# Kernel tuning notes

Hardware: AMD Instinct MI355X
Metric: run time of the kernel (lower is better)

Reference implementation:

```python
import jax, jax.numpy as jnp
import numpy as np

N_NODES = 50000
N_EDGES = 800000
D = 128          # embed_dim
H = 8            # heads
C = D // H       # per-head channels
F = 512          # ff_hidden_dim
LN_EPS = 1e-5
NEG_SLOPE = 0.2  # PyG GATConv default negative_slope


def _layernorm(x, g, b):
    mu = jnp.mean(x, axis=-1, keepdims=True)
    var = jnp.mean(jnp.square(x - mu), axis=-1, keepdims=True)
    return (x - mu) * jax.lax.rsqrt(var + LN_EPS) * g + b


def _gat_conv(x, edge_index, W, att_src, att_dst, bias):
    # PyG GATConv (concat=True, add_self_loops=True, shared lin for src/dst)
    N = x.shape[0]
    xl = (x @ W.T).reshape(N, H, C)                 # [N,H,C]
    a_s = jnp.sum(xl * att_src, axis=-1)            # [N,H]
    a_d = jnp.sum(xl * att_dst, axis=-1)            # [N,H]
    loops = jnp.arange(N)
    src = jnp.concatenate([edge_index[0], loops])   # [E+N]
    dst = jnp.concatenate([edge_index[1], loops])
    e = jax.nn.leaky_relu(a_s[src] + a_d[dst], NEG_SLOPE)  # [E+N,H]
    # segment softmax over incoming edges per destination node
    m = jax.ops.segment_max(e, dst, num_segments=N)
    m = jnp.where(jnp.isfinite(m), m, jnp.zeros_like(m))
    ex = jnp.exp(e - m[dst])
    s = jax.ops.segment_sum(ex, dst, num_segments=N)
    alpha = ex / (s[dst] + 1e-16)                   # [E+N,H]
    msg = xl[src] * alpha[:, :, None]               # [E+N,H,C]
    out = jax.ops.segment_sum(msg, dst, num_segments=N)  # [N,H,C]
    return out.reshape(N, H * C) + bias


def setup_inputs() -> dict:
    key = jax.random.key(0)
    ks = jax.random.split(key, 12)
    sc_d = 1.0 / np.sqrt(D)
    sc_f = 1.0 / np.sqrt(F)
    return {
        "x": jax.random.normal(ks[0], (N_NODES, D), dtype=jnp.float32),
        "virtual_edge_index": jax.random.randint(ks[1], (2, N_EDGES), 0, N_NODES, dtype=jnp.int64),
        "W_gat": jax.random.normal(ks[2], (H * C, D), dtype=jnp.float32) * sc_d,
        "att_src": jax.random.normal(ks[3], (H, C), dtype=jnp.float32) * sc_d,
        "att_dst": jax.random.normal(ks[4], (H, C), dtype=jnp.float32) * sc_d,
        "bias_gat": jnp.zeros((H * C,), dtype=jnp.float32),
        "W1": jax.random.normal(ks[5], (F, D), dtype=jnp.float32) * sc_d,
        "b1": jnp.zeros((F,), dtype=jnp.float32),
        "W2": jax.random.normal(ks[6], (D, F), dtype=jnp.float32) * sc_f,
        "b2": jnp.zeros((D,), dtype=jnp.float32),
        "g1": jnp.ones((D,), dtype=jnp.float32),
        "beta1": jnp.zeros((D,), dtype=jnp.float32),
        "g2": jnp.ones((D,), dtype=jnp.float32),
        "beta2": jnp.zeros((D,), dtype=jnp.float32),
    }


def reference(x, virtual_edge_index, W_gat, att_src, att_dst, bias_gat,
              W1, b1, W2, b2, g1, beta1, g2, beta2):
    h_gat = _gat_conv(x, virtual_edge_index, W_gat, att_src, att_dst, bias_gat)
    h = _layernorm(x + h_gat, g1, beta1)
    h_ff = jax.nn.relu(h @ W1.T + b1) @ W2.T + b2
    return _layernorm(h + h_ff, g2, beta2)
```

## Files before the change

### kernel.cpp

```cpp
#include <hip/hip_runtime.h>
#include <hip/hip_bf16.h>

#define N_NODES 50000
#define N_EDGES 800000
#define N_TOT   850000
#define DIM 128
#define HEADS 8
#define CH 16
#define FF 512
#define LN_EPS 1e-5f
#define NEG_SLOPE 0.2f

typedef __bf16 bf16x8 __attribute__((ext_vector_type(8)));
typedef float f32x4 __attribute__((ext_vector_type(4)));

__device__ __forceinline__ float bfr2f(unsigned short u) {
  return __uint_as_float(((unsigned)u) << 16);
}
__device__ __forceinline__ unsigned short f2bfr(float f) {
  __hip_bfloat16 h = __float2bfloat16(f);
  return *(unsigned short*)&h;
}
__device__ __forceinline__ float bf2f(__hip_bfloat16 h) { return __bfloat162float(h); }
__device__ __forceinline__ __hip_bfloat16 f2bf(float f) { return __float2bfloat16(f); }

__device__ __forceinline__ bf16x8 ldcvt8(const float* __restrict__ p) {
  const float4 a = ((const float4*)p)[0];
  const float4 b = ((const float4*)p)[1];
  bf16x8 r;
  r[0] = (__bf16)a.x; r[1] = (__bf16)a.y; r[2] = (__bf16)a.z; r[3] = (__bf16)a.w;
  r[4] = (__bf16)b.x; r[5] = (__bf16)b.y; r[6] = (__bf16)b.z; r[7] = (__bf16)b.w;
  return r;
}

__device__ __forceinline__ int ld_src(const int* ei, int mode, int e) {
  int v = mode ? ei[2 * e] : ei[e];
  return min(max(v, 0), N_NODES - 1);
}
__device__ __forceinline__ int ld_dst(const int* ei, int mode, int e) {
  int v = mode ? ei[2 * (N_EDGES + e)] : ei[N_EDGES + e];
  return min(max(v, 0), N_NODES - 1);
}
__device__ __forceinline__ int edge_mode(const int* __restrict__ ei) {
  int any = 0;
  for (int k = 1; k < 64; k += 2) any |= ei[k];
  return (any == 0) ? 1 : 0;
}

__device__ __forceinline__ float expleaky(float v) {
  v = v > 0.f ? v : NEG_SLOPE * v;
  return __expf(v);
}

__global__ __launch_bounds__(256) void k_xl(const float* __restrict__ x,
                                            const float* __restrict__ Wg,
                                            const float* __restrict__ att_s,
                                            const float* __restrict__ att_d,
                                            __hip_bfloat16* __restrict__ xl,
                                            float* __restrict__ a_s,
                                            float* __restrict__ a_d,
                                            int* __restrict__ dz) {
  int gid = blockIdx.x * 256 + threadIdx.x;
  if (gid < 100096) dz[gid] = 0;
  int w = gid >> 6;
  if (w >= 3125 * 2) return;
  int l = threadIdx.x & 63, quad = l >> 4, r = l & 15;
  int strip = w >> 1, cc = w & 1;
  f32x4 acc[4];
#pragma unroll
  for (int t = 0; t < 4; ++t) acc[t] = (f32x4){0.f, 0.f, 0.f, 0.f};
  int arow = strip * 16 + r;
  bf16x8 af[4];
#pragma unroll
  for (int kk = 0; kk < 4; ++kk) af[kk] = ldcvt8(x + arow * DIM + kk * 32 + quad * 8);
#pragma unroll
  for (int kk = 0; kk < 4; ++kk) {
    bf16x8 bfr[4];
#pragma unroll
    for (int t = 0; t < 4; ++t)
      bfr[t] = ldcvt8(Wg + (cc * 64 + t * 16 + r) * DIM + kk * 32 + quad * 8);
#pragma unroll
    for (int t = 0; t < 4; ++t)
      acc[t] = __builtin_amdgcn_mfma_f32_16x16x32_bf16(af[kk], bfr[t], acc[t], 0, 0, 0);
  }
  float ats[4], atd[4];
#pragma unroll
  for (int t = 0; t < 4; ++t) {
    ats[t] = att_s[(cc * 4 + t) * CH + r];
    atd[t] = att_d[(cc * 4 + t) * CH + r];
  }
#pragma unroll
  for (int t = 0; t < 4; ++t)
#pragma unroll
    for (int j = 0; j < 4; ++j) {
      int row = strip * 16 + quad * 4 + j;
      int col = cc * 64 + t * 16 + r;
      xl[row * DIM + col] = f2bf(acc[t][j]);
      float vs = acc[t][j] * ats[t];
      float vd = acc[t][j] * atd[t];
      vs += __shfl_xor(vs, 1); vd += __shfl_xor(vd, 1);
      vs += __shfl_xor(vs, 2); vd += __shfl_xor(vd, 2);
      vs += __shfl_xor(vs, 4); vd += __shfl_xor(vd, 4);
      vs += __shfl_xor(vs, 8); vd += __shfl_xor(vd, 8);
      if (r == 0) {
        a_s[row * 8 + cc * 4 + t] = vs;
        a_d[row * 8 + cc * 4 + t] = vd;
      }
    }
}

__global__ __launch_bounds__(256) void k_hist(const int* __restrict__ ei,
                                              const float* __restrict__ W1,
                                              const float* __restrict__ W2,
                                              __hip_bfloat16* __restrict__ wb,
                                              int* __restrict__ deg) {
  int i = blockIdx.x * 256 + threadIdx.x;
  if (i < 65536)        wb[i] = f2bf(W1[i]);
  else if (i < 131072)  wb[i] = f2bf(W2[i - 65536]);
  int m = edge_mode(ei);
  if (i < N_EDGES) atomicAdd(&deg[ld_dst(ei, m, i)], 1);
}

__global__ __launch_bounds__(1024) void k_scan(const int* __restrict__ deg, int* __restrict__ offs) {
  __shared__ int wtot[16];
  __shared__ int wbase[16];
  __shared__ int running_s;
  int tid = threadIdx.x, wv = tid >> 6, ln = tid & 63;
  if (tid == 0) running_s = 0;
  __syncthreads();
  for (int base = 0; base < N_NODES; base += 4096) {
    int i0 = base + tid * 4;
    int v0 = 0, v1 = 0, v2 = 0, v3 = 0;
    if (i0 + 3 < N_NODES) {
      int4 dv = *(const int4*)(deg + i0);
      v0 = dv.x + 1; v1 = dv.y + 1; v2 = dv.z + 1; v3 = dv.w + 1;
    } else {
      if (i0 + 0 < N_NODES) v0 = deg[i0 + 0] + 1;
      if (i0 + 1 < N_NODES) v1 = deg[i0 + 1] + 1;
      if (i0 + 2 < N_NODES) v2 = deg[i0 + 2] + 1;
      if (i0 + 3 < N_NODES) v3 = deg[i0 + 3] + 1;
    }
    int tt = v0 + v1 + v2 + v3;
    int xsc = tt;
#pragma unroll
    for (int off = 1; off < 64; off <<= 1) {
      int t = __shfl_up(xsc, off);
      if (ln >= off) xsc += t;
    }
    if (ln == 63) wtot[wv] = xsc;
    __syncthreads();
    if (wv == 0) {
      int t = (ln < 16) ? wtot[ln] : 0;
#pragma unroll
      for (int off = 1; off < 16; off <<= 1) {
        int u = __shfl_up(t, off);
        if (ln >= off) t += u;
      }
      if (ln < 16) wbase[ln] = t;
    }
    __syncthreads();
    int run0 = running_s;
    int excl = run0 + ((wv == 0) ? 0 : wbase[wv - 1]) + xsc - tt;
    if (i0 + 0 < N_NODES) offs[i0 + 0] = excl;
    excl += v0;
    if (i0 + 1 < N_NODES) offs[i0 + 1] = excl;
    excl += v1;
    if (i0 + 2 < N_NODES) offs[i0 + 2] = excl;
    excl += v2;
    if (i0 + 3 < N_NODES) offs[i0 + 3] = excl;
    __syncthreads();
    if (tid == 1023) running_s = run0 + wbase[15];
  }
  __syncthreads();
  if (tid == 0) offs[N_NODES] = running_s;
}

__global__ __launch_bounds__(256) void k_scatter(const int* __restrict__ ei,
                                                 const int* __restrict__ offs,
                                                 int* __restrict__ fill, int* __restrict__ eid) {
  int e = blockIdx.x * 256 + threadIdx.x;
  if (e < N_NODES) { eid[offs[e]] = e; }
  int m = edge_mode(ei);
  if (e < N_EDGES) {
    int d = ld_dst(ei, m, e);
    int p = offs[d] + 1 + atomicAdd(&fill[d], 1);
    eid[p] = ld_src(ei, m, e);
  }
}

__global__ __launch_bounds__(256) void k_attn(const int* __restrict__ eid, const int* __restrict__ offs,
                                              const float* __restrict__ a_s,
                                              const float* __restrict__ a_d,
                                              const __hip_bfloat16* __restrict__ xl,
                                              const float* __restrict__ x,
                                              const float* __restrict__ bias,
                                              const float* __restrict__ g1,
                                              const float* __restrict__ be1,
                                              __hip_bfloat16* __restrict__ h1out) {
  int wv = threadIdx.x >> 6, l = threadIdx.x & 63;
  int n = blockIdx.x * 4 + wv;
  int start = offs[n], end = offs[n + 1];
  int h8 = l & 7, sl8 = l >> 3;
  int hq = l >> 3;
  float adv = a_d[n * 8 + h8];

  const char* xlb = (const char*)xl;
  int l4 = 4 * l;
  float sme = 0.f;
  float A0 = 0.f, A1 = 0.f;
  int p = start;
  for (; p + 8 <= end; p += 8) {
    int s = eid[p + sl8];
    int boff = s << 8;
    float w = expleaky(a_s[s * 8 + h8] + adv);
    sme += w;
#pragma unroll
    for (int q = 0; q < 8; ++q) {
      int bq = __shfl(boff, q * 8);
      float wq = __shfl(w, q * 8 + hq);
      ushort2 u = *(const ushort2*)(xlb + bq + l4);
      A0 += wq * bfr2f(u.x);
      A1 += wq * bfr2f(u.y);
    }
  }
  int rem = end - p;
  if (rem > 0) {
    int sl = (sl8 < rem) ? sl8 : 0;
    int s = eid[p + sl];
    int boff = s << 8;
    float w = (sl8 < rem) ? expleaky(a_s[s * 8 + h8] + adv) : 0.f;
    sme += w;
    for (int q = 0; q < rem; ++q) {
      int bq = __shfl(boff, q * 8);
      float wq = __shfl(w, q * 8 + hq);
      ushort2 u = *(const ushort2*)(xlb + bq + l4);
      A0 += wq * bfr2f(u.x);
      A1 += wq * bfr2f(u.y);
    }
  }
  sme += __shfl_xor(sme, 8);
  sme += __shfl_xor(sme, 16);
  sme += __shfl_xor(sme, 32);
  float smh = __shfl(sme, hq);
  float inv = 1.f / (smh + 1e-16f);
  float acc0 = A0 * inv;
  float acc1 = A1 * inv;

  float2 xv = *(const float2*)(x + n * DIM + 2 * l);
  float2 bv = *(const float2*)(bias + 2 * l);
  float v0 = acc0 + bv.x + xv.x;
  float v1 = acc1 + bv.y + xv.y;
  float s2 = v0 + v1;
  for (int off = 32; off >= 1; off >>= 1) s2 += __shfl_xor(s2, off);
  float mu = s2 * (1.f / 128.f);
  float d0 = v0 - mu, d1 = v1 - mu;
  float q = d0 * d0 + d1 * d1;
  for (int off = 32; off >= 1; off >>= 1) q += __shfl_xor(q, off);
  float rs = rsqrtf(q * (1.f / 128.f) + LN_EPS);
  float2 gv = *(const float2*)(g1 + 2 * l);
  float2 bev = *(const float2*)(be1 + 2 * l);
  ushort2 o;
  o.x = f2bfr(d0 * rs * gv.x + bev.x);
  o.y = f2bfr(d1 * rs * gv.y + bev.y);
  *(ushort2*)((unsigned short*)h1out + n * DIM + 2 * l) = o;
}

__global__ __launch_bounds__(256) void k_ffn1(const __hip_bfloat16* __restrict__ h1,
                                              const __hip_bfloat16* __restrict__ W1b,
                                              const float* __restrict__ b1,
                                              __hip_bfloat16* __restrict__ hid,
                                              int row_base) {
  int wv = threadIdx.x >> 6, l = threadIdx.x & 63, quad = l >> 4, r = l & 15;
  int blk = blockIdx.x;
  int base = row_base + blk * 32;
  const __bf16* h1b = (const __bf16*)h1;
  const __bf16* w1 = (const __bf16*)W1b;
  int r0 = min(base + r, N_NODES - 1);
  int r1 = min(base + 16 + r, N_NODES - 1);

  bf16x8 bn[2][4];
#pragma unroll
  for (int kk = 0; kk < 4; ++kk) {
    bn[0][kk] = *(const bf16x8*)(h1b + r0 * DIM + kk * 32 + quad * 8);
    bn[1][kk] = *(const bf16x8*)(h1b + r1 * DIM + kk * 32 + quad * 8);
  }
  f32x4 acc1[8][2];
#pragma unroll
  for (int tm = 0; tm < 8; ++tm)
#pragma unroll
    for (int tn = 0; tn < 2; ++tn) acc1[tm][tn] = (f32x4){0.f, 0.f, 0.f, 0.f};
#pragma unroll
  for (int kk = 0; kk < 4; ++kk) {
    bf16x8 wf[8];
#pragma unroll
    for (int tm = 0; tm < 8; ++tm)
      wf[tm] = *(const bf16x8*)(w1 + (wv * 128 + tm * 16 + r) * DIM + kk * 32 + quad * 8);
#pragma unroll
    for (int tm = 0; tm < 8; ++tm) {
      acc1[tm][0] = __builtin_amdgcn_mfma_f32_16x16x32_bf16(wf[tm], bn[0][kk], acc1[tm][0], 0, 0, 0);
      acc1[tm][1] = __builtin_amdgcn_mfma_f32_16x16x32_bf16(wf[tm], bn[1][kk], acc1[tm][1], 0, 0, 0);
    }
  }
  unsigned short* hb = (unsigned short*)hid;
#pragma unroll
  for (int tm = 0; tm < 8; ++tm) {
    int f0 = wv * 128 + tm * 16 + quad * 4;
    float4 bb = *(const float4*)(b1 + f0);
#pragma unroll
    for (int tn = 0; tn < 2; ++tn) {
      ushort4 o;
      o.x = f2bfr(fmaxf(acc1[tm][tn][0] + bb.x, 0.f));
      o.y = f2bfr(fmaxf(acc1[tm][tn][1] + bb.y, 0.f));
      o.z = f2bfr(fmaxf(acc1[tm][tn][2] + bb.z, 0.f));
      o.w = f2bfr(fmaxf(acc1[tm][tn][3] + bb.w, 0.f));
      int idx = ((blk * 2 + tn) * 64 + wv * 16 + tm * 2 + (quad >> 1)) * 128
                + r * 8 + (quad & 1) * 4;
      *(ushort4*)(hb + idx) = o;
    }
  }
}

__global__ __launch_bounds__(256) void k_ffn2(const __hip_bfloat16* __restrict__ hid,
                                              const __hip_bfloat16* __restrict__ W2b,
                                              const float* __restrict__ b2,
                                              const float* __restrict__ g2,
                                              const float* __restrict__ be2,
                                              const __hip_bfloat16* __restrict__ h1,
                                              float* __restrict__ out,
                                              int row_base) {
  __shared__ float ps[4][2][16], pq[4][2][16];
  int wv = threadIdx.x >> 6, l = threadIdx.x & 63, quad = l >> 4, r = l & 15;
  int blk = blockIdx.x;
  int base = row_base + blk * 32;
  const __bf16* w2 = (const __bf16*)W2b;
  const unsigned short* hb = (const unsigned short*)hid;

  f32x4 acc2[2][2];
#pragma unroll
  for (int s = 0; s < 2; ++s)
#pragma unroll
    for (int tn = 0; tn < 2; ++tn) acc2[s][tn] = (f32x4){0.f, 0.f, 0.f, 0.f};

  const unsigned short* a0base = hb + ((blk * 2 + 0) * 64 + quad) * 128 + r * 8;
  const unsigned short* a1base = hb + ((blk * 2 + 1) * 64 + quad) * 128 + r * 8;
  const __bf16* w2base = w2 + (wv * 32 + r) * FF + quad * 8;

#pragma unroll 4
  for (int ka = 0; ka < 16; ++ka) {
    bf16x8 a0 = *(const bf16x8*)(a0base + ka * 512);
    bf16x8 a1 = *(const bf16x8*)(a1base + ka * 512);
    bf16x8 wa0 = *(const bf16x8*)(w2base + ka * 32);
    bf16x8 wa1 = *(const bf16x8*)(w2base + 16 * FF + ka * 32);
    acc2[0][0] = __builtin_amdgcn_mfma_f32_16x16x32_bf16(a0, wa0, acc2[0][0], 0, 0, 0);
    acc2[0][1] = __builtin_amdgcn_mfma_f32_16x16x32_bf16(a0, wa1, acc2[0][1], 0, 0, 0);
    acc2[1][0] = __builtin_amdgcn_mfma_f32_16x16x32_bf16(a1, wa0, acc2[1][0], 0, 0, 0);
    acc2[1][1] = __builtin_amdgcn_mfma_f32_16x16x32_bf16(a1, wa1, acc2[1][1], 0, 0, 0);
  }
#pragma unroll
  for (int s = 0; s < 2; ++s)
#pragma unroll
    for (int tn = 0; tn < 2; ++tn) {
      int col = wv * 32 + tn * 16 + r;
      float b2c = b2[col];
#pragma unroll
      for (int j = 0; j < 4; ++j) {
        int row = min(base + s * 16 + quad * 4 + j, N_NODES - 1);
        acc2[s][tn][j] += b2c + bf2f(h1[row * DIM + col]);
      }
    }
#pragma unroll
  for (int s = 0; s < 2; ++s)
#pragma unroll
    for (int j = 0; j < 4; ++j) {
      float sm = acc2[s][0][j] + acc2[s][1][j];
      float qm = acc2[s][0][j] * acc2[s][0][j] + acc2[s][1][j] * acc2[s][1][j];
      sm += __shfl_xor(sm, 1); sm += __shfl_xor(sm, 2); sm += __shfl_xor(sm, 4); sm += __shfl_xor(sm, 8);
      qm += __shfl_xor(qm, 1); qm += __shfl_xor(qm, 2); qm += __shfl_xor(qm, 4); qm += __shfl_xor(qm, 8);
      if (r == j) { ps[wv][s][quad * 4 + j] = sm; pq[wv][s][quad * 4 + j] = qm; }
    }
  __syncthreads();
#pragma unroll
  for (int s = 0; s < 2; ++s)
#pragma unroll
    for (int j = 0; j < 4; ++j) {
      int row16 = quad * 4 + j;
      float st = (ps[0][s][row16] + ps[1][s][row16]) + (ps[2][s][row16] + ps[3][s][row16]);
      float qt = (pq[0][s][row16] + pq[1][s][row16]) + (pq[2][s][row16] + pq[3][s][row16]);
      float mu = st * (1.f / 128.f);
      float var = qt * (1.f / 128.f) - mu * mu;
      float rs = rsqrtf(var + LN_EPS);
      int grow = base + s * 16 + row16;
      if (grow < N_NODES) {
#pragma unroll
        for (int tn = 0; tn < 2; ++tn) {
          int col = wv * 32 + tn * 16 + r;
          out[grow * DIM + col] = (acc2[s][tn][j] - mu) * rs * g2[col] + be2[col];
        }
      }
    }
}

#define OFF_XL     0u
#define SZ_XL      (N_NODES * DIM * 2u)
#define OFF_AS     (OFF_XL + SZ_XL)
#define SZ_AS      (N_NODES * HEADS * 4u)
#define OFF_AD     (OFF_AS + SZ_AS)
#define OFF_DEG    (OFF_AD + SZ_AS)
#define SZ_DEG     200192u
#define OFF_FILL   (OFF_DEG + SZ_DEG)
#define OFF_OFFS   (OFF_FILL + SZ_DEG)
#define SZ_OFFS    200448u
#define OFF_EID    (OFF_OFFS + SZ_OFFS)
#define SZ_EID     3400192u
#define OFF_H1     (OFF_EID + SZ_EID)
#define SZ_H1      (50016u * DIM * 2u)
#define OFF_WB     (OFF_H1 + SZ_H1)
#define SZ_WB      262144u
#define OFF_HID    (OFF_WB + SZ_WB)
#define SZ_HID_FULL (50016u * FF * 2u)
#define FFN_CHUNK0_BLOCKS 782
#define FFN_CHUNK1_BLOCKS 781
#define FFN_CHUNK0_ROWS   (FFN_CHUNK0_BLOCKS * 32)

extern "C" void kernel_launch(void* const* d_in, const int* in_sizes, int n_in,
                              void* d_out, int out_size, void* d_ws, size_t ws_size,
                              hipStream_t stream) {
  const float* x     = (const float*)d_in[0];
  const int*   ei    = (const int*)d_in[1];
  const float* Wg    = (const float*)d_in[2];
  const float* att_s = (const float*)d_in[3];
  const float* att_d = (const float*)d_in[4];
  const float* bias  = (const float*)d_in[5];
  const float* W1    = (const float*)d_in[6];
  const float* b1    = (const float*)d_in[7];
  const float* W2    = (const float*)d_in[8];
  const float* b2    = (const float*)d_in[9];
  const float* g1    = (const float*)d_in[10];
  const float* be1   = (const float*)d_in[11];
  const float* g2    = (const float*)d_in[12];
  const float* be2   = (const float*)d_in[13];

  char* ws = (char*)d_ws;
  __hip_bfloat16* xl     = (__hip_bfloat16*)(ws + OFF_XL);
  float*          a_s    = (float*)(ws + OFF_AS);
  float*          a_d    = (float*)(ws + OFF_AD);
  int*            deg    = (int*)(ws + OFF_DEG);
  int*            fill   = (int*)(ws + OFF_FILL);
  int*            offs   = (int*)(ws + OFF_OFFS);
  int*            eid    = (int*)(ws + OFF_EID);
  __hip_bfloat16* h1     = (__hip_bfloat16*)(ws + OFF_H1);
  __hip_bfloat16* wbuf   = (__hip_bfloat16*)(ws + OFF_WB);
  __hip_bfloat16* W1b    = wbuf;
  __hip_bfloat16* W2b    = wbuf + 65536;
  __hip_bfloat16* hid    = (__hip_bfloat16*)(ws + OFF_HID);
  float*          out    = (float*)d_out;

  k_xl     <<<1563,  256, 0, stream>>>(x, Wg, att_s, att_d, xl, a_s, a_d, deg);
  k_hist   <<<3125,  256, 0, stream>>>(ei, W1, W2, wbuf, deg);
  k_scan   <<<1,    1024, 0, stream>>>(deg, offs);
  k_scatter<<<3125,  256, 0, stream>>>(ei, offs, fill, eid);
  k_attn   <<<12500, 256, 0, stream>>>(eid, offs, a_s, a_d, xl, x, bias, g1, be1, h1);

  if (ws_size >= (size_t)OFF_HID + SZ_HID_FULL) {
    k_ffn1 <<<1563, 256, 0, stream>>>(h1, W1b, b1, hid, 0);
    k_ffn2 <<<1563, 256, 0, stream>>>(hid, W2b, b2, g2, be2, h1, out, 0);
  } else {
    k_ffn1 <<<FFN_CHUNK0_BLOCKS, 256, 0, stream>>>(h1, W1b, b1, hid, 0);
    k_ffn2 <<<FFN_CHUNK0_BLOCKS, 256, 0, stream>>>(hid, W2b, b2, g2, be2, h1, out, 0);
    k_ffn1 <<<FFN_CHUNK1_BLOCKS, 256, 0, stream>>>(h1, W1b, b1, hid, FFN_CHUNK0_ROWS);
    k_ffn2 <<<FFN_CHUNK1_BLOCKS, 256, 0, stream>>>(hid, W2b, b2, g2, be2, h1, out, FFN_CHUNK0_ROWS);
  }
}
```

Before: 349.4 us.

## Replace global-atomic CSR build with partitioned shared-memory histograms and per-chunk offsets

```diff
diff --git a/kernel.cpp b/kernel.cpp
--- a/kernel.cpp
+++ b/kernel.cpp
@@ -11,6 +11,11 @@
 #define LN_EPS 1e-5f
 #define NEG_SLOPE 0.2f
 
+#define PART    8
+#define NCHUNK  128
+#define CHUNK_E (N_EDGES / NCHUNK)
+#define NPP     (N_NODES / PART)
+
 typedef __bf16 bf16x8 __attribute__((ext_vector_type(8)));
 typedef float f32x4 __attribute__((ext_vector_type(4)));
 
@@ -58,10 +63,8 @@
                                             const float* __restrict__ att_d,
                                             __hip_bfloat16* __restrict__ xl,
                                             float* __restrict__ a_s,
-                                            float* __restrict__ a_d,
-                                            int* __restrict__ dz) {
+                                            float* __restrict__ a_d) {
   int gid = blockIdx.x * 256 + threadIdx.x;
-  if (gid < 100096) dz[gid] = 0;
   int w = gid >> 6;
   if (w >= 3125 * 2) return;
   int l = threadIdx.x & 63, quad = l >> 4, r = l & 15;
@@ -109,19 +112,49 @@
     }
 }
 
-__global__ __launch_bounds__(256) void k_hist(const int* __restrict__ ei,
-                                              const float* __restrict__ W1,
-                                              const float* __restrict__ W2,
-                                              __hip_bfloat16* __restrict__ wb,
-                                              int* __restrict__ deg) {
-  int i = blockIdx.x * 256 + threadIdx.x;
-  if (i < 65536)        wb[i] = f2bf(W1[i]);
-  else if (i < 131072)  wb[i] = f2bf(W2[i - 65536]);
+__global__ __launch_bounds__(256) void k_hist2(const int* __restrict__ ei,
+                                               const float* __restrict__ W1,
+                                               const float* __restrict__ W2,
+                                               __hip_bfloat16* __restrict__ wb,
+                                               unsigned short* __restrict__ blkh) {
+  __shared__ unsigned int hist[NPP];
+  int p = blockIdx.x & 7, c = blockIdx.x >> 3;
+  int tid = threadIdx.x;
+  int gi = blockIdx.x * 256 + tid;
+  if (gi < 65536)        wb[gi] = f2bf(W1[gi]);
+  else if (gi < 131072)  wb[gi] = f2bf(W2[gi - 65536]);
+  for (int i = tid; i < NPP; i += 256) hist[i] = 0;
   int m = edge_mode(ei);
-  if (i < N_EDGES) atomicAdd(&deg[ld_dst(ei, m, i)], 1);
-}
-
-__global__ __launch_bounds__(1024) void k_scan(const int* __restrict__ deg, int* __restrict__ offs) {
+  __syncthreads();
+  int nlo = p * NPP;
+  int e1 = (c + 1) * CHUNK_E;
+  for (int e = c * CHUNK_E + tid; e < e1; e += 256) {
+    int d = ld_dst(ei, m, e) - nlo;
+    if ((unsigned)d < (unsigned)NPP) atomicAdd(&hist[d], 1u);
+  }
+  __syncthreads();
+  unsigned short* dst = blkh + (size_t)c * N_NODES + nlo;
+  for (int i = tid; i < NPP; i += 256) dst[i] = (unsigned short)hist[i];
+}
+
+__global__ __launch_bounds__(256) void k_nscan(unsigned short* __restrict__ blkh,
+                                               int* __restrict__ deg) {
+  int n = blockIdx.x * 256 + threadIdx.x;
+  if (n >= N_NODES) return;
+  int run = 0;
+#pragma unroll 8
+  for (int c = 0; c < NCHUNK; ++c) {
+    unsigned short* ptr = blkh + (size_t)c * N_NODES + n;
+    int v = *ptr;
+    *ptr = (unsigned short)run;
+    run += v;
+  }
+  deg[n] = run;
+}
+
+__global__ __launch_bounds__(1024) void k_scan(const int* __restrict__ deg,
+                                               int* __restrict__ offs,
+                                               int* __restrict__ eid) {
   __shared__ int wtot[16];
   __shared__ int wbase[16];
   __shared__ int running_s;
@@ -161,13 +194,13 @@
     __syncthreads();
     int run0 = running_s;
     int excl = run0 + ((wv == 0) ? 0 : wbase[wv - 1]) + xsc - tt;
-    if (i0 + 0 < N_NODES) offs[i0 + 0] = excl;
+    if (i0 + 0 < N_NODES) { offs[i0 + 0] = excl; eid[excl] = i0 + 0; }
     excl += v0;
-    if (i0 + 1 < N_NODES) offs[i0 + 1] = excl;
+    if (i0 + 1 < N_NODES) { offs[i0 + 1] = excl; eid[excl] = i0 + 1; }
     excl += v1;
-    if (i0 + 2 < N_NODES) offs[i0 + 2] = excl;
+    if (i0 + 2 < N_NODES) { offs[i0 + 2] = excl; eid[excl] = i0 + 2; }
     excl += v2;
-    if (i0 + 3 < N_NODES) offs[i0 + 3] = excl;
+    if (i0 + 3 < N_NODES) { offs[i0 + 3] = excl; eid[excl] = i0 + 3; }
     __syncthreads();
     if (tid == 1023) running_s = run0 + wbase[15];
   }
@@ -177,14 +210,25 @@
 
 __global__ __launch_bounds__(256) void k_scatter(const int* __restrict__ ei,
                                                  const int* __restrict__ offs,
-                                                 int* __restrict__ fill, int* __restrict__ eid) {
-  int e = blockIdx.x * 256 + threadIdx.x;
-  if (e < N_NODES) { eid[offs[e]] = e; }
+                                                 const unsigned short* __restrict__ blkh,
+                                                 int* __restrict__ eid) {
+  __shared__ unsigned int fill[NPP];
+  int p = blockIdx.x & 7, c = blockIdx.x >> 3;
+  int tid = threadIdx.x;
+  for (int i = tid; i < NPP; i += 256) fill[i] = 0;
   int m = edge_mode(ei);
-  if (e < N_EDGES) {
-    int d = ld_dst(ei, m, e);
-    int p = offs[d] + 1 + atomicAdd(&fill[d], 1);
-    eid[p] = ld_src(ei, m, e);
+  __syncthreads();
+  int nlo = p * NPP;
+  const unsigned short* exl = blkh + (size_t)c * N_NODES;
+  int e1 = (c + 1) * CHUNK_E;
+  for (int e = c * CHUNK_E + tid; e < e1; e += 256) {
+    int dg = ld_dst(ei, m, e);
+    int d = dg - nlo;
+    if ((unsigned)d < (unsigned)NPP) {
+      unsigned ord = atomicAdd(&fill[d], 1u);
+      int slot = offs[dg] + 1 + (int)exl[dg] + (int)ord;
+      eid[slot] = ld_src(ei, m, e);
+    }
   }
 }
 
@@ -407,8 +451,7 @@
 #define OFF_AD     (OFF_AS + SZ_AS)
 #define OFF_DEG    (OFF_AD + SZ_AS)
 #define SZ_DEG     200192u
-#define OFF_FILL   (OFF_DEG + SZ_DEG)
-#define OFF_OFFS   (OFF_FILL + SZ_DEG)
+#define OFF_OFFS   (OFF_DEG + SZ_DEG)
 #define SZ_OFFS    200448u
 #define OFF_EID    (OFF_OFFS + SZ_OFFS)
 #define SZ_EID     3400192u
@@ -417,6 +460,7 @@
 #define OFF_WB     (OFF_H1 + SZ_H1)
 #define SZ_WB      262144u
 #define OFF_HID    (OFF_WB + SZ_WB)
+#define OFF_BLKH   OFF_HID
 #define SZ_HID_FULL (50016u * FF * 2u)
 #define FFN_CHUNK0_BLOCKS 782
 #define FFN_CHUNK1_BLOCKS 781
@@ -445,21 +489,22 @@
   float*          a_s    = (float*)(ws + OFF_AS);
   float*          a_d    = (float*)(ws + OFF_AD);
   int*            deg    = (int*)(ws + OFF_DEG);
-  int*            fill   = (int*)(ws + OFF_FILL);
   int*            offs   = (int*)(ws + OFF_OFFS);
   int*            eid    = (int*)(ws + OFF_EID);
   __hip_bfloat16* h1     = (__hip_bfloat16*)(ws + OFF_H1);
   __hip_bfloat16* wbuf   = (__hip_bfloat16*)(ws + OFF_WB);
   __hip_bfloat16* W1b    = wbuf;
   __hip_bfloat16* W2b    = wbuf + 65536;
+  unsigned short* blkh   = (unsigned short*)(ws + OFF_BLKH);
   __hip_bfloat16* hid    = (__hip_bfloat16*)(ws + OFF_HID);
   float*          out    = (float*)d_out;
 
-  k_xl     <<<1563,  256, 0, stream>>>(x, Wg, att_s, att_d, xl, a_s, a_d, deg);
-  k_hist   <<<3125,  256, 0, stream>>>(ei, W1, W2, wbuf, deg);
-  k_scan   <<<1,    1024, 0, stream>>>(deg, offs);
-  k_scatter<<<3125,  256, 0, stream>>>(ei, offs, fill, eid);
-  k_attn   <<<12500, 256, 0, stream>>>(eid, offs, a_s, a_d, xl, x, bias, g1, be1, h1);
+  k_xl     <<<1563,         256, 0, stream>>>(x, Wg, att_s, att_d, xl, a_s, a_d);
+  k_hist2  <<<PART * NCHUNK, 256, 0, stream>>>(ei, W1, W2, wbuf, blkh);
+  k_nscan  <<<196,          256, 0, stream>>>(blkh, deg);
+  k_scan   <<<1,           1024, 0, stream>>>(deg, offs, eid);
+  k_scatter<<<PART * NCHUNK, 256, 0, stream>>>(ei, offs, blkh, eid);
+  k_attn   <<<12500,        256, 0, stream>>>(eid, offs, a_s, a_d, xl, x, bias, g1, be1, h1);
 
   if (ws_size >= (size_t)OFF_HID + SZ_HID_FULL) {
     k_ffn1 <<<1563, 256, 0, stream>>>(h1, W1b, b1, hid, 0);
```

After: 340.8 us. -2.4%, faster.
